# Kernel tuning notes

Measured on AMD Instinct MI355X. Metric: run time of the kernel, lower is better.

Reference implementation:

```python
import jax, jax.numpy as jnp
import numpy as np


def setup_inputs() -> dict:
    key = jax.random.key(0)
    ks = jax.random.split(key, 5)
    S, B, H, L = 512, 64, 1024, 2
    scale = 0.1
    return {
        "x": jax.random.normal(ks[0], (S, B, H), dtype=jnp.float32),
        "h0": jnp.zeros((L, B, H), dtype=jnp.float32),
        "c0": jnp.zeros((L, B, H), dtype=jnp.float32),
        "Wx": jax.random.uniform(ks[1], (L, 4 * H, H), minval=-scale, maxval=scale, dtype=jnp.float32),
        "Wh": jax.random.uniform(ks[2], (L, 4 * H, H), minval=-scale, maxval=scale, dtype=jnp.float32),
        "bx": jax.random.uniform(ks[3], (L, 4 * H), minval=-scale, maxval=scale, dtype=jnp.float32),
        "bh": jax.random.uniform(ks[4], (L, 4 * H), minval=-scale, maxval=scale, dtype=jnp.float32),
    }


def _cell(x_t, h_prev, c_prev, Wx_l, Wh_l, bx_l, bh_l, H):
    # gates: [B, 4H]; chunk order per source: f, i, o, c_ex
    gates = x_t @ Wx_l.T + bx_l + h_prev @ Wh_l.T + bh_l
    f, i, o, c_ex = jnp.split(gates, 4, axis=1)
    f = jax.nn.sigmoid(f)
    i = jax.nn.sigmoid(i)
    o = jax.nn.sigmoid(o)
    c_ex = jnp.tanh(c_ex)
    c = f * c_prev + i * c_ex
    h = o * jnp.tanh(c)
    return h, c


def reference(x, h0, c0, Wx, Wh, bx, bh):
    # x: [S, B, H]; h0/c0: [L, B, H]; Wx/Wh: [L, 4H, H]; bx/bh: [L, 4H]
    L = h0.shape[0]
    H = h0.shape[-1]

    def step(carry, x_t):
        h_all, c_all = carry  # each [L, B, H]
        out = x_t
        hs, cs = [], []
        for l in range(L):  # small fixed layer count
            h, c = _cell(out, h_all[l], c_all[l], Wx[l], Wh[l], bx[l], bh[l], H)
            out = h  # dropout is identity in eval mode
            hs.append(h)
            cs.append(c)
        return (jnp.stack(hs, 0), jnp.stack(cs, 0)), out

    (h_fin, c_fin), ys = jax.lax.scan(step, (h0, c0), x)
    return ys, (h_fin, c_fin)
```

## Files before the change

### kernel.cpp

```cpp
#include <hip/hip_runtime.h>

typedef __bf16 bf16_t;
typedef __bf16 bf16x8 __attribute__((ext_vector_type(8)));
typedef __bf16 bf16x4 __attribute__((ext_vector_type(4)));
typedef float  f32x4  __attribute__((ext_vector_type(4)));
typedef unsigned long long u64;

#define S_LEN 512
#define BATCH 64
#define HID 1024
#define BH (BATCH*HID)
#define G4 (4*HID)
#define NBLK 256
#define LBLK 128
#define NTHR 512
#define CSTRIDE 32

__device__ __forceinline__ float sigmoid_f(float x) { return 1.f / (1.f + __expf(-x)); }
__device__ __forceinline__ float tanh_f(float x) {
    float e = __expf(-2.f * fabsf(x));
    float t = (1.f - e) / (1.f + e);
    return x >= 0.f ? t : -t;
}

__device__ __forceinline__ bf16x8 cvt8(const float* p) {
    float4 a = *reinterpret_cast<const float4*>(p);
    float4 b = *reinterpret_cast<const float4*>(p + 4);
    bf16x8 r;
    r[0] = (bf16_t)a.x; r[1] = (bf16_t)a.y; r[2] = (bf16_t)a.z; r[3] = (bf16_t)a.w;
    r[4] = (bf16_t)b.x; r[5] = (bf16_t)b.y; r[6] = (bf16_t)b.z; r[7] = (bf16_t)b.w;
    return r;
}

__device__ __forceinline__ void wait_words(const unsigned* dw, int cc, unsigned thr, int lane) {
    const unsigned* p = dw + (size_t)(16 * cc + (lane & 15)) * CSTRIDE;
    for (;;) {
        unsigned v = thr;
        if (lane < 16)
            v = __hip_atomic_load(p, __ATOMIC_RELAXED, __HIP_MEMORY_SCOPE_AGENT);
        if (__all((int)(v >= thr))) break;
        __builtin_amdgcn_s_sleep(1);
    }
    asm volatile("" ::: "memory");
}

__device__ __forceinline__ void gemm_phase_chunked(
    const bf16_t* __restrict__ abase, const unsigned* __restrict__ dwords, unsigned thr,
    int grbase, const unsigned char* __restrict__ lds_w,
    int kh, int quad, int r16, int lane, int ff, f32x4& acc0, f32x4& acc1)
{
    bf16x8 af[8];
    wait_words(dwords, 4 * kh, thr, lane);
    if (!ff) __builtin_amdgcn_fence(__ATOMIC_ACQUIRE, "agent");
    #pragma unroll
    for (int j = 0; j < 4; ++j)
        af[j] = *reinterpret_cast<const bf16x8*>(abase + j * 32);
    #pragma unroll
    for (int c = 0; c < 4; ++c) {
        if (c < 3) {
            wait_words(dwords, 4 * kh + c + 1, thr, lane);
            if (!ff) __builtin_amdgcn_fence(__ATOMIC_ACQUIRE, "agent");
            #pragma unroll
            for (int j = 0; j < 4; ++j)
                af[((c + 1) & 1) * 4 + j] =
                    *reinterpret_cast<const bf16x8*>(abase + (4 * (c + 1) + j) * 32);
        }
        #pragma unroll
        for (int j = 0; j < 4; ++j) {
            int ks = 4 * c + j;
            int gr = grbase + kh * 64 + ks * 4 + quad;
            bf16x8 b0 = *reinterpret_cast<const bf16x8*>(&lds_w[gr * 512 + r16 * 16]);
            bf16x8 b1 = *reinterpret_cast<const bf16x8*>(&lds_w[gr * 512 + (16 + r16) * 16]);
            acc0 = __builtin_amdgcn_mfma_f32_16x16x32_bf16(af[(c & 1) * 4 + j], b0, acc0, 0, 0, 0);
            acc1 = __builtin_amdgcn_mfma_f32_16x16x32_bf16(af[(c & 1) * 4 + j], b1, acc1, 0, 0, 0);
        }
    }
}

__global__ void prep_kernel(const float* __restrict__ h0,
                            bf16_t* __restrict__ h0buf, bf16_t* __restrict__ h1buf,
                            unsigned* __restrict__ dw, int mask0, int mask1) {
    int gtid = blockIdx.x * blockDim.x + threadIdx.x;
    int gsz  = gridDim.x * blockDim.x;
    if (gtid < 2 * LBLK) dw[gtid * CSTRIDE] = 0u;
    for (int i = gtid; i < BH; i += gsz) {
        h0buf[(size_t)mask0 * BH + i] = (bf16_t)h0[i];
        h1buf[(size_t)mask1 * BH + i] = (bf16_t)h0[BH + i];
    }
}

__global__ __launch_bounds__(NTHR, 2) void lstm_persistent(
    const float* __restrict__ x,
    const float* __restrict__ c0,
    const float* __restrict__ Wx,
    const float* __restrict__ Wh,
    const float* __restrict__ bx,
    const float* __restrict__ bh,
    float* __restrict__ out,
    bf16_t* __restrict__ h0buf,
    bf16_t* __restrict__ h1buf,
    unsigned* __restrict__ dw,
    int ff, int mask0, int mask1)
{
    __shared__ __attribute__((aligned(16))) unsigned char lds_w[256 * 512];
    __shared__ __attribute__((aligned(16))) float lds_red[8 * 256];
    __shared__ __attribute__((aligned(16))) float lds_hf[BATCH * 8];

    const int tid  = threadIdx.x;
    const int bid  = blockIdx.x;
    const int l    = bid >> 7;
    const int ug8  = bid & 127;
    const int lane = tid & 63;
    const int wv   = tid >> 6;
    const int mt   = wv >> 1;
    const int kh   = wv & 1;
    const int quad = lane >> 4;
    const int r16  = lane & 15;

    float* ys   = out;
    float* hfin = out + (size_t)S_LEN * BH;
    float* cfin = hfin + 2 * BH;

    {
        const float* WxL = Wx + (size_t)l * G4 * HID;
        const float* WhL = Wh + (size_t)l * G4 * HID;
        for (int ch = tid; ch < 32 * 256; ch += NTHR) {
            int row = ch & 31;
            int gr  = ch >> 5;
            int ul = row >> 2, g = row & 3;
            size_t R = (size_t)g * HID + 8 * ug8 + ul;
            const float* src = (gr < 128) ? (WxL + R * HID + (size_t)gr * 8)
                                          : (WhL + R * HID + (size_t)(gr - 128) * 8);
            *reinterpret_cast<bf16x8*>(&lds_w[gr * 512 + row * 16]) = cvt8(src);
        }
    }

    const int b_loc  = lane >> 2;
    const int uu     = lane & 3;
    const int b_glob = 16 * mt + b_loc;
    const int u_loc  = 4 * kh + uu;
    const int u_glob = 8 * ug8 + u_loc;

    float bias_r[4];
    #pragma unroll
    for (int gi = 0; gi < 4; ++gi) {
        int R = gi * HID + u_glob;
        bias_r[gi] = bx[l * G4 + R] + bh[l * G4 + R];
    }
    float c_reg = c0[(size_t)l * BH + (size_t)b_glob * HID + u_glob];

    bf16_t* pubbuf = (l == 0) ? h0buf : h1buf;
    const int pubmask = (l == 0) ? mask0 : mask1;
    const unsigned* dw0 = dw;
    const unsigned* dw1 = dw + LBLK * CSTRIDE;
    unsigned* myword = &dw[(l * LBLK + ug8) * CSTRIDE];
    __syncthreads();

    const int arow_off = (16 * mt + r16) * HID + kh * 512 + quad * 8;

    bf16x8 axp[16];
    if (l == 0) {
        const float* arow = x + arow_off;
        #pragma unroll
        for (int ks = 0; ks < 16; ++ks) axp[ks] = cvt8(arow + ks * 32);
    }

    for (int t = 0; t < S_LEN; ++t) {
        f32x4 acc0 = {0.f, 0.f, 0.f, 0.f};
        f32x4 acc1 = {0.f, 0.f, 0.f, 0.f};

        if (l == 0) {
            #pragma unroll
            for (int ks = 0; ks < 16; ++ks) {
                int gr = kh * 64 + ks * 4 + quad;
                bf16x8 b0 = *reinterpret_cast<const bf16x8*>(&lds_w[gr * 512 + r16 * 16]);
                bf16x8 b1 = *reinterpret_cast<const bf16x8*>(&lds_w[gr * 512 + (16 + r16) * 16]);
                acc0 = __builtin_amdgcn_mfma_f32_16x16x32_bf16(axp[ks], b0, acc0, 0, 0, 0);
                acc1 = __builtin_amdgcn_mfma_f32_16x16x32_bf16(axp[ks], b1, acc1, 0, 0, 0);
            }
            const bf16_t* ah = h0buf + (size_t)((t - 1) & mask0) * BH + arow_off;
            gemm_phase_chunked(ah, dw0, (unsigned)t, 128, lds_w,
                               kh, quad, r16, lane, ff, acc0, acc1);
        } else {
            const bf16_t* ah = h1buf + (size_t)((t - 1) & mask1) * BH + arow_off;
            gemm_phase_chunked(ah, dw1, (unsigned)t, 128, lds_w,
                               kh, quad, r16, lane, ff, acc0, acc1);
            const bf16_t* ax = h0buf + (size_t)(t & mask0) * BH + arow_off;
            gemm_phase_chunked(ax, dw0, (unsigned)(t + 1), 0, lds_w,
                               kh, quad, r16, lane, ff, acc0, acc1);
        }

        {
            f32x4 ship = kh ? acc0 : acc1;
            *reinterpret_cast<f32x4*>(&lds_red[wv * 256 + lane * 4]) = ship;
            __syncthreads();
            f32x4 part = *reinterpret_cast<const f32x4*>(&lds_red[(wv ^ 1) * 256 + lane * 4]);
            f32x4 keep = kh ? acc1 : acc0;
            acc0 = keep + part;
        }

        {
            const int quad_s = b_loc >> 2;
            const int reg_s  = b_loc & 3;
            float gsum[4];
            #pragma unroll
            for (int gi = 0; gi < 4; ++gi) {
                int lane_s = (quad_s << 4) | (4 * uu + gi);
                float v0 = __shfl(acc0[0], lane_s, 64);
                float v1 = __shfl(acc0[1], lane_s, 64);
                float v2 = __shfl(acc0[2], lane_s, 64);
                float v3 = __shfl(acc0[3], lane_s, 64);
                float v  = (reg_s == 0) ? v0 : (reg_s == 1) ? v1 : (reg_s == 2) ? v2 : v3;
                gsum[gi] = v + bias_r[gi];
            }
            float fg = sigmoid_f(gsum[0]);
            float ig = sigmoid_f(gsum[1]);
            float og = sigmoid_f(gsum[2]);
            float cx = tanh_f(gsum[3]);
            float cN = fg * c_reg + ig * cx;
            float h  = og * tanh_f(cN);
            c_reg = cN;
            lds_hf[b_glob * 8 + u_loc] = h;
            if (t == S_LEN - 1) {
                hfin[(size_t)l * BH + (size_t)b_glob * HID + u_glob] = h;
                cfin[(size_t)l * BH + (size_t)b_glob * HID + u_glob] = cN;
            }
        }
        __syncthreads();

        if (tid < 64) {
            if (!ff && l == 0 && t >= 8) {
                const unsigned thr = (unsigned)(t - 6);
                for (;;) {
                    unsigned v0 = __hip_atomic_load(&dw1[lane * CSTRIDE],
                                                    __ATOMIC_RELAXED, __HIP_MEMORY_SCOPE_AGENT);
                    unsigned v1 = __hip_atomic_load(&dw1[(64 + lane) * CSTRIDE],
                                                    __ATOMIC_RELAXED, __HIP_MEMORY_SCOPE_AGENT);
                    if (__all((int)(v0 >= thr && v1 >= thr))) break;
                    __builtin_amdgcn_s_sleep(1);
                }
            }
            const float* hp = &lds_hf[lane * 8];
            union { bf16x4 v; u64 q; } p0, p1;
            #pragma unroll
            for (int j = 0; j < 4; ++j) {
                p0.v[j] = (bf16_t)hp[j];
                p1.v[j] = (bf16_t)hp[4 + j];
            }
            bf16_t* dst = pubbuf + (size_t)(t & pubmask) * BH + (size_t)lane * HID + 8 * ug8;
            __hip_atomic_store((u64*)(void*)dst,       p0.q, __ATOMIC_RELAXED, __HIP_MEMORY_SCOPE_AGENT);
            __hip_atomic_store((u64*)(void*)(dst + 4), p1.q, __ATOMIC_RELAXED, __HIP_MEMORY_SCOPE_AGENT);
            asm volatile("s_waitcnt vmcnt(0)" ::: "memory");
            if (lane == 0)
                __hip_atomic_store(myword, (unsigned)(t + 1),
                                   __ATOMIC_RELAXED, __HIP_MEMORY_SCOPE_AGENT);
            if (l == 1) {
                float* yd = ys + (size_t)t * BH + (size_t)lane * HID + 8 * ug8;
                __builtin_nontemporal_store(*reinterpret_cast<const f32x4*>(hp),     reinterpret_cast<f32x4*>(yd));
                __builtin_nontemporal_store(*reinterpret_cast<const f32x4*>(hp + 4), reinterpret_cast<f32x4*>(yd + 4));
            }
        }

        if (l == 0 && t + 1 < S_LEN) {
            const float* arow = x + (size_t)(t + 1) * BH + arow_off;
            #pragma unroll
            for (int ks = 0; ks < 16; ++ks) axp[ks] = cvt8(arow + ks * 32);
        }
    }
}

extern "C" void kernel_launch(void* const* d_in, const int* in_sizes, int n_in,
                              void* d_out, int out_size, void* d_ws, size_t ws_size,
                              hipStream_t stream) {
    (void)in_sizes; (void)n_in; (void)out_size;
    const float* x  = (const float*)d_in[0];
    const float* h0 = (const float*)d_in[1];
    const float* c0 = (const float*)d_in[2];
    const float* Wx = (const float*)d_in[3];
    const float* Wh = (const float*)d_in[4];
    const float* bx = (const float*)d_in[5];
    const float* bh = (const float*)d_in[6];

    unsigned char* ws = (unsigned char*)d_ws;
    unsigned* dw = (unsigned*)ws;
    size_t off = 32768;
    size_t need_ff = off + (size_t)2 * S_LEN * BH * 2;
    int ff, mask0, mask1;
    bf16_t *h0buf, *h1buf;
    if (ws_size >= need_ff) {
        ff = 1; mask0 = S_LEN - 1; mask1 = S_LEN - 1;
        h0buf = (bf16_t*)(ws + off); off += (size_t)S_LEN * BH * 2;
        h1buf = (bf16_t*)(ws + off);
    } else {
        ff = 0; mask0 = 7; mask1 = 1;
        h0buf = (bf16_t*)(ws + off); off += (size_t)8 * BH * 2;
        h1buf = (bf16_t*)(ws + off);
    }

    prep_kernel<<<2048, 256, 0, stream>>>(h0, h0buf, h1buf, dw, mask0, mask1);
    lstm_persistent<<<NBLK, NTHR, 0, stream>>>(x, c0, Wx, Wh, bx, bh, (float*)d_out,
                                               h0buf, h1buf, dw, ff, mask0, mask1);
}
```

Baseline: 6.470 ms.

## Replace block-wide barriers with per-wave flags and per-wave publish

Removes both __syncthreads per timestep. The K-split partial-sum exchange now uses LDS producer/consumer flags between wave pairs, and each wave publishes its own h slice to global memory with its own ready flag. Consumers therefore wait on finer-grained per-wave counters (32 lanes polled) instead of one counter per block. The intent is to cut barrier stalls and let waves run ahead independently. In exchange there are more flag words to poll, spin-waits in LDS, and riskier memory ordering.

New measurement: 7.107 ms. +9.8%, slower.

```diff
diff --git a/kernel.cpp b/kernel.cpp
--- a/kernel.cpp
+++ b/kernel.cpp
@@ -2,7 +2,6 @@
 
 typedef __bf16 bf16_t;
 typedef __bf16 bf16x8 __attribute__((ext_vector_type(8)));
-typedef __bf16 bf16x4 __attribute__((ext_vector_type(4)));
 typedef float  f32x4  __attribute__((ext_vector_type(4)));
 typedef unsigned long long u64;
 
@@ -14,7 +13,7 @@
 #define NBLK 256
 #define LBLK 128
 #define NTHR 512
-#define CSTRIDE 32
+#define CSTRIDE 8
 
 __device__ __forceinline__ float sigmoid_f(float x) { return 1.f / (1.f + __expf(-x)); }
 __device__ __forceinline__ float tanh_f(float x) {
@@ -32,11 +31,10 @@
     return r;
 }
 
-__device__ __forceinline__ void wait_words(const unsigned* dw, int cc, unsigned thr, int lane) {
-    const unsigned* p = dw + (size_t)(16 * cc + (lane & 15)) * CSTRIDE;
+__device__ __forceinline__ void wait32(const unsigned* p, unsigned thr, int lane) {
     for (;;) {
         unsigned v = thr;
-        if (lane < 16)
+        if (lane < 32)
             v = __hip_atomic_load(p, __ATOMIC_RELAXED, __HIP_MEMORY_SCOPE_AGENT);
         if (__all((int)(v >= thr))) break;
         __builtin_amdgcn_s_sleep(1);
@@ -44,13 +42,13 @@
     asm volatile("" ::: "memory");
 }
 
-__device__ __forceinline__ void gemm_phase_chunked(
-    const bf16_t* __restrict__ abase, const unsigned* __restrict__ dwords, unsigned thr,
+__device__ __forceinline__ void gemm_phase(
+    const bf16_t* __restrict__ abase, const unsigned* __restrict__ pl, unsigned thr,
     int grbase, const unsigned char* __restrict__ lds_w,
     int kh, int quad, int r16, int lane, int ff, f32x4& acc0, f32x4& acc1)
 {
     bf16x8 af[8];
-    wait_words(dwords, 4 * kh, thr, lane);
+    wait32(pl + (size_t)(4 * kh) * (16 * 8 * CSTRIDE), thr, lane);
     if (!ff) __builtin_amdgcn_fence(__ATOMIC_ACQUIRE, "agent");
     #pragma unroll
     for (int j = 0; j < 4; ++j)
@@ -58,7 +56,7 @@
     #pragma unroll
     for (int c = 0; c < 4; ++c) {
         if (c < 3) {
-            wait_words(dwords, 4 * kh + c + 1, thr, lane);
+            wait32(pl + (size_t)(4 * kh + c + 1) * (16 * 8 * CSTRIDE), thr, lane);
             if (!ff) __builtin_amdgcn_fence(__ATOMIC_ACQUIRE, "agent");
             #pragma unroll
             for (int j = 0; j < 4; ++j)
@@ -82,7 +80,7 @@
                             unsigned* __restrict__ dw, int mask0, int mask1) {
     int gtid = blockIdx.x * blockDim.x + threadIdx.x;
     int gsz  = gridDim.x * blockDim.x;
-    if (gtid < 2 * LBLK) dw[gtid * CSTRIDE] = 0u;
+    if (gtid < 2048) dw[gtid * CSTRIDE] = 0u;
     for (int i = gtid; i < BH; i += gsz) {
         h0buf[(size_t)mask0 * BH + i] = (bf16_t)h0[i];
         h1buf[(size_t)mask1 * BH + i] = (bf16_t)h0[BH + i];
@@ -104,7 +102,8 @@
 {
     __shared__ __attribute__((aligned(16))) unsigned char lds_w[256 * 512];
     __shared__ __attribute__((aligned(16))) float lds_red[8 * 256];
-    __shared__ __attribute__((aligned(16))) float lds_hf[BATCH * 8];
+    __shared__ unsigned lds_prod[8];
+    __shared__ unsigned lds_rdf[8];
 
     const int tid  = threadIdx.x;
     const int bid  = blockIdx.x;
@@ -120,6 +119,8 @@
     float* ys   = out;
     float* hfin = out + (size_t)S_LEN * BH;
     float* cfin = hfin + 2 * BH;
+
+    if (tid < 8) { lds_prod[tid] = 0u; lds_rdf[tid] = 0u; }
 
     {
         const float* WxL = Wx + (size_t)l * G4 * HID;
@@ -151,9 +152,11 @@
 
     bf16_t* pubbuf = (l == 0) ? h0buf : h1buf;
     const int pubmask = (l == 0) ? mask0 : mask1;
-    const unsigned* dw0 = dw;
-    const unsigned* dw1 = dw + LBLK * CSTRIDE;
-    unsigned* myword = &dw[(l * LBLK + ug8) * CSTRIDE];
+    const int lblk = lane & 15;
+    const int lkhp = (lane >> 4) & 1;
+    const unsigned* pl0 = dw + (size_t)(0 * 1024 + lblk * 8 + mt * 2 + lkhp) * CSTRIDE;
+    const unsigned* pl1 = dw + (size_t)(1 * 1024 + lblk * 8 + mt * 2 + lkhp) * CSTRIDE;
+    unsigned* myword = dw + (size_t)(l * 1024 + ug8 * 8 + mt * 2 + kh) * CSTRIDE;
     __syncthreads();
 
     const int arow_off = (16 * mt + r16) * HID + kh * 512 + quad * 8;
@@ -179,26 +182,38 @@
                 acc1 = __builtin_amdgcn_mfma_f32_16x16x32_bf16(axp[ks], b1, acc1, 0, 0, 0);
             }
             const bf16_t* ah = h0buf + (size_t)((t - 1) & mask0) * BH + arow_off;
-            gemm_phase_chunked(ah, dw0, (unsigned)t, 128, lds_w,
-                               kh, quad, r16, lane, ff, acc0, acc1);
+            gemm_phase(ah, pl0, (unsigned)t, 128, lds_w, kh, quad, r16, lane, ff, acc0, acc1);
         } else {
             const bf16_t* ah = h1buf + (size_t)((t - 1) & mask1) * BH + arow_off;
-            gemm_phase_chunked(ah, dw1, (unsigned)t, 128, lds_w,
-                               kh, quad, r16, lane, ff, acc0, acc1);
+            gemm_phase(ah, pl1, (unsigned)t, 128, lds_w, kh, quad, r16, lane, ff, acc0, acc1);
             const bf16_t* ax = h0buf + (size_t)(t & mask0) * BH + arow_off;
-            gemm_phase_chunked(ax, dw0, (unsigned)(t + 1), 0, lds_w,
-                               kh, quad, r16, lane, ff, acc0, acc1);
+            gemm_phase(ax, pl0, (unsigned)(t + 1), 0, lds_w, kh, quad, r16, lane, ff, acc0, acc1);
         }
 
         {
+            const unsigned gen = (unsigned)(t + 1);
+            while (__hip_atomic_load(&lds_rdf[mt * 2 + kh], __ATOMIC_RELAXED,
+                                     __HIP_MEMORY_SCOPE_WORKGROUP) < (unsigned)t) {}
             f32x4 ship = kh ? acc0 : acc1;
-            *reinterpret_cast<f32x4*>(&lds_red[wv * 256 + lane * 4]) = ship;
-            __syncthreads();
-            f32x4 part = *reinterpret_cast<const f32x4*>(&lds_red[(wv ^ 1) * 256 + lane * 4]);
+            *reinterpret_cast<f32x4*>(&lds_red[(mt * 2 + kh) * 256 + lane * 4]) = ship;
+            __builtin_amdgcn_fence(__ATOMIC_RELEASE, "workgroup");
+            if (lane == 0)
+                __hip_atomic_store(&lds_prod[mt * 2 + kh], gen, __ATOMIC_RELAXED,
+                                   __HIP_MEMORY_SCOPE_WORKGROUP);
+            while (__hip_atomic_load(&lds_prod[mt * 2 + (kh ^ 1)], __ATOMIC_RELAXED,
+                                     __HIP_MEMORY_SCOPE_WORKGROUP) < gen) {}
+            __builtin_amdgcn_fence(__ATOMIC_ACQUIRE, "workgroup");
+            f32x4 part = *reinterpret_cast<const f32x4*>(
+                &lds_red[(mt * 2 + (kh ^ 1)) * 256 + lane * 4]);
             f32x4 keep = kh ? acc1 : acc0;
             acc0 = keep + part;
-        }
-
+            asm volatile("s_waitcnt lgkmcnt(0)" ::: "memory");
+            if (lane == 0)
+                __hip_atomic_store(&lds_rdf[mt * 2 + (kh ^ 1)], gen, __ATOMIC_RELAXED,
+                                   __HIP_MEMORY_SCOPE_WORKGROUP);
+        }
+
+        float h, cN;
         {
             const int quad_s = b_loc >> 2;
             const int reg_s  = b_loc & 3;
@@ -217,48 +232,67 @@
             float ig = sigmoid_f(gsum[1]);
             float og = sigmoid_f(gsum[2]);
             float cx = tanh_f(gsum[3]);
-            float cN = fg * c_reg + ig * cx;
-            float h  = og * tanh_f(cN);
+            cN = fg * c_reg + ig * cx;
+            h  = og * tanh_f(cN);
             c_reg = cN;
-            lds_hf[b_glob * 8 + u_loc] = h;
-            if (t == S_LEN - 1) {
-                hfin[(size_t)l * BH + (size_t)b_glob * HID + u_glob] = h;
-                cfin[(size_t)l * BH + (size_t)b_glob * HID + u_glob] = cN;
-            }
-        }
-        __syncthreads();
-
-        if (tid < 64) {
-            if (!ff && l == 0 && t >= 8) {
+        }
+
+        if (!ff) {
+            if (l == 0 && t >= 8) {
                 const unsigned thr = (unsigned)(t - 6);
+                const unsigned* b0p = dw + (size_t)(1024 + lane * 8 + mt * 2) * CSTRIDE;
+                const unsigned* b1p = dw + (size_t)(1024 + (lane + 64) * 8 + mt * 2) * CSTRIDE;
                 for (;;) {
-                    unsigned v0 = __hip_atomic_load(&dw1[lane * CSTRIDE],
-                                                    __ATOMIC_RELAXED, __HIP_MEMORY_SCOPE_AGENT);
-                    unsigned v1 = __hip_atomic_load(&dw1[(64 + lane) * CSTRIDE],
-                                                    __ATOMIC_RELAXED, __HIP_MEMORY_SCOPE_AGENT);
-                    if (__all((int)(v0 >= thr && v1 >= thr))) break;
+                    unsigned a0 = __hip_atomic_load(b0p,           __ATOMIC_RELAXED, __HIP_MEMORY_SCOPE_AGENT);
+                    unsigned a1 = __hip_atomic_load(b0p + CSTRIDE, __ATOMIC_RELAXED, __HIP_MEMORY_SCOPE_AGENT);
+                    unsigned c0w = __hip_atomic_load(b1p,           __ATOMIC_RELAXED, __HIP_MEMORY_SCOPE_AGENT);
+                    unsigned c1w = __hip_atomic_load(b1p + CSTRIDE, __ATOMIC_RELAXED, __HIP_MEMORY_SCOPE_AGENT);
+                    if (__all((int)(a0 >= thr && a1 >= thr && c0w >= thr && c1w >= thr))) break;
                     __builtin_amdgcn_s_sleep(1);
                 }
             }
-            const float* hp = &lds_hf[lane * 8];
-            union { bf16x4 v; u64 q; } p0, p1;
-            #pragma unroll
-            for (int j = 0; j < 4; ++j) {
-                p0.v[j] = (bf16_t)hp[j];
-                p1.v[j] = (bf16_t)hp[4 + j];
-            }
-            bf16_t* dst = pubbuf + (size_t)(t & pubmask) * BH + (size_t)lane * HID + 8 * ug8;
-            __hip_atomic_store((u64*)(void*)dst,       p0.q, __ATOMIC_RELAXED, __HIP_MEMORY_SCOPE_AGENT);
-            __hip_atomic_store((u64*)(void*)(dst + 4), p1.q, __ATOMIC_RELAXED, __HIP_MEMORY_SCOPE_AGENT);
+            if (l == 1 && t >= 2) {
+                const unsigned thr = (unsigned)t;
+                const unsigned* b0p = dw + (size_t)(1024 + lane * 8 + mt * 2) * CSTRIDE;
+                const unsigned* b1p = dw + (size_t)(1024 + (lane + 64) * 8 + mt * 2) * CSTRIDE;
+                for (;;) {
+                    unsigned a0 = __hip_atomic_load(b0p,           __ATOMIC_RELAXED, __HIP_MEMORY_SCOPE_AGENT);
+                    unsigned a1 = __hip_atomic_load(b0p + CSTRIDE, __ATOMIC_RELAXED, __HIP_MEMORY_SCOPE_AGENT);
+                    unsigned c0w = __hip_atomic_load(b1p,           __ATOMIC_RELAXED, __HIP_MEMORY_SCOPE_AGENT);
+                    unsigned c1w = __hip_atomic_load(b1p + CSTRIDE, __ATOMIC_RELAXED, __HIP_MEMORY_SCOPE_AGENT);
+                    if (__all((int)(a0 >= thr && a1 >= thr && c0w >= thr && c1w >= thr))) break;
+                    __builtin_amdgcn_s_sleep(1);
+                }
+            }
+            asm volatile("" ::: "memory");
+        }
+
+        {
+            union { bf16_t b; unsigned short s; } cvb; cvb.b = (bf16_t)h;
+            unsigned lo  = (unsigned)cvb.s;
+            unsigned x1  = (unsigned)__shfl_xor((int)lo, 1, 64);
+            unsigned p32 = lo | (x1 << 16);
+            unsigned p32o = (unsigned)__shfl_xor((int)p32, 2, 64);
+            u64 q = (u64)p32 | ((u64)p32o << 32);
+            if (uu == 0) {
+                bf16_t* dst = pubbuf + (size_t)(t & pubmask) * BH
+                            + (size_t)b_glob * HID + 8 * ug8 + 4 * kh;
+                __hip_atomic_store((u64*)(void*)dst, q, __ATOMIC_RELAXED,
+                                   __HIP_MEMORY_SCOPE_AGENT);
+            }
             asm volatile("s_waitcnt vmcnt(0)" ::: "memory");
             if (lane == 0)
-                __hip_atomic_store(myword, (unsigned)(t + 1),
-                                   __ATOMIC_RELAXED, __HIP_MEMORY_SCOPE_AGENT);
-            if (l == 1) {
-                float* yd = ys + (size_t)t * BH + (size_t)lane * HID + 8 * ug8;
-                __builtin_nontemporal_store(*reinterpret_cast<const f32x4*>(hp),     reinterpret_cast<f32x4*>(yd));
-                __builtin_nontemporal_store(*reinterpret_cast<const f32x4*>(hp + 4), reinterpret_cast<f32x4*>(yd + 4));
-            }
+                __hip_atomic_store(myword, (unsigned)(t + 1), __ATOMIC_RELAXED,
+                                   __HIP_MEMORY_SCOPE_AGENT);
+        }
+
+        if (l == 1) {
+            float* yd = ys + (size_t)t * BH + (size_t)b_glob * HID + u_glob;
+            __builtin_nontemporal_store(h, yd);
+        }
+        if (t == S_LEN - 1) {
+            hfin[(size_t)l * BH + (size_t)b_glob * HID + u_glob] = h;
+            cfin[(size_t)l * BH + (size_t)b_glob * HID + u_glob] = cN;
         }
 
         if (l == 0 && t + 1 < S_LEN) {
@@ -283,7 +317,7 @@
 
     unsigned char* ws = (unsigned char*)d_ws;
     unsigned* dw = (unsigned*)ws;
-    size_t off = 32768;
+    size_t off = 2048 * CSTRIDE * sizeof(unsigned);
     size_t need_ff = off + (size_t)2 * S_LEN * BH * 2;
     int ff, mask0, mask1;
     bf16_t *h0buf, *h1buf;
```

## Inline chunked recurrent GEMM, merge layer-1 phases, prefetch next x earlier

Applied to the files above, without the earlier changes.

The chunked GEMM helper is inlined, and layer 1 now runs its two phases (own h, then layer-0 h) as one eight-chunk loop. This lets the next chunk's A-fragment load and flag wait overlap across the phase boundary. Layer 0 now issues the next step's x load and bf16 conversion right after the input MFMAs, so it overlaps the spin-wait on the recurrent flags instead of sitting after the publish. The flag-word stride is halved, putting the counters in fewer cache lines and possibly adding contention between pollers and writers. Keeping the prefetched x values live longer raises register pressure.

Result: slower. 6.640 ms (+2.6%).

```diff
diff --git a/kernel.cpp b/kernel.cpp
--- a/kernel.cpp
+++ b/kernel.cpp
@@ -14,7 +14,7 @@
 #define NBLK 256
 #define LBLK 128
 #define NTHR 512
-#define CSTRIDE 32
+#define CSTRIDE 16
 
 __device__ __forceinline__ float sigmoid_f(float x) { return 1.f / (1.f + __expf(-x)); }
 __device__ __forceinline__ float tanh_f(float x) {
@@ -32,8 +32,8 @@
     return r;
 }
 
-__device__ __forceinline__ void wait_words(const unsigned* dw, int cc, unsigned thr, int lane) {
-    const unsigned* p = dw + (size_t)(16 * cc + (lane & 15)) * CSTRIDE;
+__device__ __forceinline__ void wait_words(const unsigned* dwl, int cc, unsigned thr, int lane) {
+    const unsigned* p = dwl + (size_t)(16 * cc + (lane & 15)) * CSTRIDE;
     for (;;) {
         unsigned v = thr;
         if (lane < 16)
@@ -42,39 +42,6 @@
         __builtin_amdgcn_s_sleep(1);
     }
     asm volatile("" ::: "memory");
-}
-
-__device__ __forceinline__ void gemm_phase_chunked(
-    const bf16_t* __restrict__ abase, const unsigned* __restrict__ dwords, unsigned thr,
-    int grbase, const unsigned char* __restrict__ lds_w,
-    int kh, int quad, int r16, int lane, int ff, f32x4& acc0, f32x4& acc1)
-{
-    bf16x8 af[8];
-    wait_words(dwords, 4 * kh, thr, lane);
-    if (!ff) __builtin_amdgcn_fence(__ATOMIC_ACQUIRE, "agent");
-    #pragma unroll
-    for (int j = 0; j < 4; ++j)
-        af[j] = *reinterpret_cast<const bf16x8*>(abase + j * 32);
-    #pragma unroll
-    for (int c = 0; c < 4; ++c) {
-        if (c < 3) {
-            wait_words(dwords, 4 * kh + c + 1, thr, lane);
-            if (!ff) __builtin_amdgcn_fence(__ATOMIC_ACQUIRE, "agent");
-            #pragma unroll
-            for (int j = 0; j < 4; ++j)
-                af[((c + 1) & 1) * 4 + j] =
-                    *reinterpret_cast<const bf16x8*>(abase + (4 * (c + 1) + j) * 32);
-        }
-        #pragma unroll
-        for (int j = 0; j < 4; ++j) {
-            int ks = 4 * c + j;
-            int gr = grbase + kh * 64 + ks * 4 + quad;
-            bf16x8 b0 = *reinterpret_cast<const bf16x8*>(&lds_w[gr * 512 + r16 * 16]);
-            bf16x8 b1 = *reinterpret_cast<const bf16x8*>(&lds_w[gr * 512 + (16 + r16) * 16]);
-            acc0 = __builtin_amdgcn_mfma_f32_16x16x32_bf16(af[(c & 1) * 4 + j], b0, acc0, 0, 0, 0);
-            acc1 = __builtin_amdgcn_mfma_f32_16x16x32_bf16(af[(c & 1) * 4 + j], b1, acc1, 0, 0, 0);
-        }
-    }
 }
 
 __global__ void prep_kernel(const float* __restrict__ h0,
@@ -178,16 +145,77 @@
                 acc0 = __builtin_amdgcn_mfma_f32_16x16x32_bf16(axp[ks], b0, acc0, 0, 0, 0);
                 acc1 = __builtin_amdgcn_mfma_f32_16x16x32_bf16(axp[ks], b1, acc1, 0, 0, 0);
             }
+            if (t + 1 < S_LEN) {
+                const float* arow = x + (size_t)(t + 1) * BH + arow_off;
+                #pragma unroll
+                for (int ks = 0; ks < 16; ++ks) axp[ks] = cvt8(arow + ks * 32);
+            }
             const bf16_t* ah = h0buf + (size_t)((t - 1) & mask0) * BH + arow_off;
-            gemm_phase_chunked(ah, dw0, (unsigned)t, 128, lds_w,
-                               kh, quad, r16, lane, ff, acc0, acc1);
+            bf16x8 af[8];
+            wait_words(dw0, 4 * kh, (unsigned)t, lane);
+            if (!ff) __builtin_amdgcn_fence(__ATOMIC_ACQUIRE, "agent");
+            #pragma unroll
+            for (int j = 0; j < 4; ++j)
+                af[j] = *reinterpret_cast<const bf16x8*>(ah + j * 32);
+            #pragma unroll
+            for (int c = 0; c < 4; ++c) {
+                if (c < 3) {
+                    wait_words(dw0, 4 * kh + c + 1, (unsigned)t, lane);
+                    if (!ff) __builtin_amdgcn_fence(__ATOMIC_ACQUIRE, "agent");
+                    #pragma unroll
+                    for (int j = 0; j < 4; ++j)
+                        af[((c + 1) & 1) * 4 + j] =
+                            *reinterpret_cast<const bf16x8*>(ah + (4 * (c + 1) + j) * 32);
+                }
+                #pragma unroll
+                for (int j = 0; j < 4; ++j) {
+                    int ks = 4 * c + j;
+                    int gr = 128 + kh * 64 + ks * 4 + quad;
+                    bf16x8 b0 = *reinterpret_cast<const bf16x8*>(&lds_w[gr * 512 + r16 * 16]);
+                    bf16x8 b1 = *reinterpret_cast<const bf16x8*>(&lds_w[gr * 512 + (16 + r16) * 16]);
+                    acc0 = __builtin_amdgcn_mfma_f32_16x16x32_bf16(af[(c & 1) * 4 + j], b0, acc0, 0, 0, 0);
+                    acc1 = __builtin_amdgcn_mfma_f32_16x16x32_bf16(af[(c & 1) * 4 + j], b1, acc1, 0, 0, 0);
+                }
+            }
         } else {
             const bf16_t* ah = h1buf + (size_t)((t - 1) & mask1) * BH + arow_off;
-            gemm_phase_chunked(ah, dw1, (unsigned)t, 128, lds_w,
-                               kh, quad, r16, lane, ff, acc0, acc1);
             const bf16_t* ax = h0buf + (size_t)(t & mask0) * BH + arow_off;
-            gemm_phase_chunked(ax, dw0, (unsigned)(t + 1), 0, lds_w,
-                               kh, quad, r16, lane, ff, acc0, acc1);
+            bf16x8 af[8];
+            wait_words(dw1, 4 * kh, (unsigned)t, lane);
+            if (!ff) __builtin_amdgcn_fence(__ATOMIC_ACQUIRE, "agent");
+            #pragma unroll
+            for (int j = 0; j < 4; ++j)
+                af[j] = *reinterpret_cast<const bf16x8*>(ah + j * 32);
+            #pragma unroll
+            for (int c = 0; c < 8; ++c) {
+                if (c < 7) {
+                    const int cn = c + 1;
+                    if (cn < 4) {
+                        wait_words(dw1, 4 * kh + cn, (unsigned)t, lane);
+                        if (!ff) __builtin_amdgcn_fence(__ATOMIC_ACQUIRE, "agent");
+                        #pragma unroll
+                        for (int j = 0; j < 4; ++j)
+                            af[(cn & 1) * 4 + j] =
+                                *reinterpret_cast<const bf16x8*>(ah + (4 * cn + j) * 32);
+                    } else {
+                        wait_words(dw0, 4 * kh + (cn - 4), (unsigned)(t + 1), lane);
+                        if (!ff) __builtin_amdgcn_fence(__ATOMIC_ACQUIRE, "agent");
+                        #pragma unroll
+                        for (int j = 0; j < 4; ++j)
+                            af[(cn & 1) * 4 + j] =
+                                *reinterpret_cast<const bf16x8*>(ax + (4 * (cn - 4) + j) * 32);
+                    }
+                }
+                #pragma unroll
+                for (int j = 0; j < 4; ++j) {
+                    int ks = 4 * (c & 3) + j;
+                    int gr = ((c < 4) ? 128 : 0) + kh * 64 + ks * 4 + quad;
+                    bf16x8 b0 = *reinterpret_cast<const bf16x8*>(&lds_w[gr * 512 + r16 * 16]);
+                    bf16x8 b1 = *reinterpret_cast<const bf16x8*>(&lds_w[gr * 512 + (16 + r16) * 16]);
+                    acc0 = __builtin_amdgcn_mfma_f32_16x16x32_bf16(af[(c & 1) * 4 + j], b0, acc0, 0, 0, 0);
+                    acc1 = __builtin_amdgcn_mfma_f32_16x16x32_bf16(af[(c & 1) * 4 + j], b1, acc1, 0, 0, 0);
+                }
+            }
         }
 
         {
@@ -259,12 +287,6 @@
                 __builtin_nontemporal_store(*reinterpret_cast<const f32x4*>(hp),     reinterpret_cast<f32x4*>(yd));
                 __builtin_nontemporal_store(*reinterpret_cast<const f32x4*>(hp + 4), reinterpret_cast<f32x4*>(yd + 4));
             }
-        }
-
-        if (l == 0 && t + 1 < S_LEN) {
-            const float* arow = x + (size_t)(t + 1) * BH + arow_off;
-            #pragma unroll
-            for (int ks = 0; ks < 16; ++ks) axp[ks] = cvt8(arow + ks * 32);
         }
     }
 }
```

## Replace chunked per-slice waits with single full-layer flag waits and prefetch x earlier

Applied to the files above, without the earlier changes.

Drops the chunked wait-then-load pipeline, where each quarter of K waited on its own 16 producer flags. Each wave now polls all 128 layer flags at once (layer 1 waits on both layers together) and then loads the whole h slice into registers before the MFMA loop. The flag stride is halved, and layer 0 prefetches the next x row before the h wait instead of at the end of the step. This cuts polling round trips and fences and hides x load latency, at the cost of losing overlap between early chunks and late producers and using more registers.

After: 6.746 ms. +4.3%, slower.

```diff
diff --git a/kernel.cpp b/kernel.cpp
--- a/kernel.cpp
+++ b/kernel.cpp
@@ -14,7 +14,7 @@
 #define NBLK 256
 #define LBLK 128
 #define NTHR 512
-#define CSTRIDE 32
+#define CSTRIDE 16
 
 __device__ __forceinline__ float sigmoid_f(float x) { return 1.f / (1.f + __expf(-x)); }
 __device__ __forceinline__ float tanh_f(float x) {
@@ -32,49 +32,33 @@
     return r;
 }
 
-__device__ __forceinline__ void wait_words(const unsigned* dw, int cc, unsigned thr, int lane) {
-    const unsigned* p = dw + (size_t)(16 * cc + (lane & 15)) * CSTRIDE;
+__device__ __forceinline__ void wait_layer(const unsigned* w, unsigned thr, int lane) {
+    const unsigned* p0 = w + (size_t)lane * CSTRIDE;
+    const unsigned* p1 = w + (size_t)(64 + lane) * CSTRIDE;
     for (;;) {
-        unsigned v = thr;
-        if (lane < 16)
-            v = __hip_atomic_load(p, __ATOMIC_RELAXED, __HIP_MEMORY_SCOPE_AGENT);
-        if (__all((int)(v >= thr))) break;
+        unsigned a = __hip_atomic_load(p0, __ATOMIC_RELAXED, __HIP_MEMORY_SCOPE_AGENT);
+        unsigned b = __hip_atomic_load(p1, __ATOMIC_RELAXED, __HIP_MEMORY_SCOPE_AGENT);
+        if (__all((int)(a >= thr && b >= thr))) break;
         __builtin_amdgcn_s_sleep(1);
     }
     asm volatile("" ::: "memory");
 }
 
-__device__ __forceinline__ void gemm_phase_chunked(
-    const bf16_t* __restrict__ abase, const unsigned* __restrict__ dwords, unsigned thr,
-    int grbase, const unsigned char* __restrict__ lds_w,
-    int kh, int quad, int r16, int lane, int ff, f32x4& acc0, f32x4& acc1)
-{
-    bf16x8 af[8];
-    wait_words(dwords, 4 * kh, thr, lane);
-    if (!ff) __builtin_amdgcn_fence(__ATOMIC_ACQUIRE, "agent");
-    #pragma unroll
-    for (int j = 0; j < 4; ++j)
-        af[j] = *reinterpret_cast<const bf16x8*>(abase + j * 32);
-    #pragma unroll
-    for (int c = 0; c < 4; ++c) {
-        if (c < 3) {
-            wait_words(dwords, 4 * kh + c + 1, thr, lane);
-            if (!ff) __builtin_amdgcn_fence(__ATOMIC_ACQUIRE, "agent");
-            #pragma unroll
-            for (int j = 0; j < 4; ++j)
-                af[((c + 1) & 1) * 4 + j] =
-                    *reinterpret_cast<const bf16x8*>(abase + (4 * (c + 1) + j) * 32);
-        }
-        #pragma unroll
-        for (int j = 0; j < 4; ++j) {
-            int ks = 4 * c + j;
-            int gr = grbase + kh * 64 + ks * 4 + quad;
-            bf16x8 b0 = *reinterpret_cast<const bf16x8*>(&lds_w[gr * 512 + r16 * 16]);
-            bf16x8 b1 = *reinterpret_cast<const bf16x8*>(&lds_w[gr * 512 + (16 + r16) * 16]);
-            acc0 = __builtin_amdgcn_mfma_f32_16x16x32_bf16(af[(c & 1) * 4 + j], b0, acc0, 0, 0, 0);
-            acc1 = __builtin_amdgcn_mfma_f32_16x16x32_bf16(af[(c & 1) * 4 + j], b1, acc1, 0, 0, 0);
-        }
-    }
+__device__ __forceinline__ void wait_dual(const unsigned* w0, unsigned thr0,
+                                          const unsigned* w1, unsigned thr1, int lane) {
+    const unsigned* p00 = w0 + (size_t)lane * CSTRIDE;
+    const unsigned* p01 = w0 + (size_t)(64 + lane) * CSTRIDE;
+    const unsigned* p10 = w1 + (size_t)lane * CSTRIDE;
+    const unsigned* p11 = w1 + (size_t)(64 + lane) * CSTRIDE;
+    for (;;) {
+        unsigned a = __hip_atomic_load(p00, __ATOMIC_RELAXED, __HIP_MEMORY_SCOPE_AGENT);
+        unsigned b = __hip_atomic_load(p01, __ATOMIC_RELAXED, __HIP_MEMORY_SCOPE_AGENT);
+        unsigned c = __hip_atomic_load(p10, __ATOMIC_RELAXED, __HIP_MEMORY_SCOPE_AGENT);
+        unsigned d = __hip_atomic_load(p11, __ATOMIC_RELAXED, __HIP_MEMORY_SCOPE_AGENT);
+        if (__all((int)(a >= thr0 && b >= thr0 && c >= thr1 && d >= thr1))) break;
+        __builtin_amdgcn_s_sleep(1);
+    }
+    asm volatile("" ::: "memory");
 }
 
 __global__ void prep_kernel(const float* __restrict__ h0,
@@ -178,16 +162,54 @@
                 acc0 = __builtin_amdgcn_mfma_f32_16x16x32_bf16(axp[ks], b0, acc0, 0, 0, 0);
                 acc1 = __builtin_amdgcn_mfma_f32_16x16x32_bf16(axp[ks], b1, acc1, 0, 0, 0);
             }
+            if (t + 1 < S_LEN) {
+                const float* arow = x + (size_t)(t + 1) * BH + arow_off;
+                #pragma unroll
+                for (int ks = 0; ks < 16; ++ks) axp[ks] = cvt8(arow + ks * 32);
+            }
+            wait_layer(dw0, (unsigned)t, lane);
+            if (!ff) __builtin_amdgcn_fence(__ATOMIC_ACQUIRE, "agent");
             const bf16_t* ah = h0buf + (size_t)((t - 1) & mask0) * BH + arow_off;
-            gemm_phase_chunked(ah, dw0, (unsigned)t, 128, lds_w,
-                               kh, quad, r16, lane, ff, acc0, acc1);
+            bf16x8 af[16];
+            #pragma unroll
+            for (int ks = 0; ks < 16; ++ks)
+                af[ks] = *reinterpret_cast<const bf16x8*>(ah + ks * 32);
+            #pragma unroll
+            for (int ks = 0; ks < 16; ++ks) {
+                int gr = 128 + kh * 64 + ks * 4 + quad;
+                bf16x8 b0 = *reinterpret_cast<const bf16x8*>(&lds_w[gr * 512 + r16 * 16]);
+                bf16x8 b1 = *reinterpret_cast<const bf16x8*>(&lds_w[gr * 512 + (16 + r16) * 16]);
+                acc0 = __builtin_amdgcn_mfma_f32_16x16x32_bf16(af[ks], b0, acc0, 0, 0, 0);
+                acc1 = __builtin_amdgcn_mfma_f32_16x16x32_bf16(af[ks], b1, acc1, 0, 0, 0);
+            }
         } else {
+            wait_dual(dw0, (unsigned)(t + 1), dw1, (unsigned)t, lane);
+            if (!ff) __builtin_amdgcn_fence(__ATOMIC_ACQUIRE, "agent");
             const bf16_t* ah = h1buf + (size_t)((t - 1) & mask1) * BH + arow_off;
-            gemm_phase_chunked(ah, dw1, (unsigned)t, 128, lds_w,
-                               kh, quad, r16, lane, ff, acc0, acc1);
             const bf16_t* ax = h0buf + (size_t)(t & mask0) * BH + arow_off;
-            gemm_phase_chunked(ax, dw0, (unsigned)(t + 1), 0, lds_w,
-                               kh, quad, r16, lane, ff, acc0, acc1);
+            bf16x8 ahf[16], axf[16];
+            #pragma unroll
+            for (int ks = 0; ks < 16; ++ks)
+                ahf[ks] = *reinterpret_cast<const bf16x8*>(ah + ks * 32);
+            #pragma unroll
+            for (int ks = 0; ks < 16; ++ks)
+                axf[ks] = *reinterpret_cast<const bf16x8*>(ax + ks * 32);
+            #pragma unroll
+            for (int ks = 0; ks < 16; ++ks) {
+                int gr = 128 + kh * 64 + ks * 4 + quad;
+                bf16x8 b0 = *reinterpret_cast<const bf16x8*>(&lds_w[gr * 512 + r16 * 16]);
+                bf16x8 b1 = *reinterpret_cast<const bf16x8*>(&lds_w[gr * 512 + (16 + r16) * 16]);
+                acc0 = __builtin_amdgcn_mfma_f32_16x16x32_bf16(ahf[ks], b0, acc0, 0, 0, 0);
+                acc1 = __builtin_amdgcn_mfma_f32_16x16x32_bf16(ahf[ks], b1, acc1, 0, 0, 0);
+            }
+            #pragma unroll
+            for (int ks = 0; ks < 16; ++ks) {
+                int gr = kh * 64 + ks * 4 + quad;
+                bf16x8 b0 = *reinterpret_cast<const bf16x8*>(&lds_w[gr * 512 + r16 * 16]);
+                bf16x8 b1 = *reinterpret_cast<const bf16x8*>(&lds_w[gr * 512 + (16 + r16) * 16]);
+                acc0 = __builtin_amdgcn_mfma_f32_16x16x32_bf16(axf[ks], b0, acc0, 0, 0, 0);
+                acc1 = __builtin_amdgcn_mfma_f32_16x16x32_bf16(axf[ks], b1, acc1, 0, 0, 0);
+            }
         }
 
         {
@@ -259,12 +281,6 @@
                 __builtin_nontemporal_store(*reinterpret_cast<const f32x4*>(hp),     reinterpret_cast<f32x4*>(yd));
                 __builtin_nontemporal_store(*reinterpret_cast<const f32x4*>(hp + 4), reinterpret_cast<f32x4*>(yd + 4));
             }
-        }
-
-        if (l == 0 && t + 1 < S_LEN) {
-            const float* arow = x + (size_t)(t + 1) * BH + arow_off;
-            #pragma unroll
-            for (int ks = 0; ks < 16; ++ks) axp[ks] = cvt8(arow + ks * 32);
         }
     }
 }
```
